# Kernel tuning notes

Measured on AMD Instinct MI355X. Metric: run time of the kernel, lower is better.

The kernel has to match this reference:

```python
import jax, jax.numpy as jnp
import numpy as np
from jax import lax

E = 8      # embed dim
H = 8      # num heads (head_dim = 1)
EPS = 1e-5


def pe_row(pos, d=E):
    # PositionalEncoding quirk: original adds pe[:, x.size(1), :] -> a SINGLE row at index L.
    i = jnp.arange(0, d, 2, dtype=jnp.float32)
    div = jnp.exp(i * (-np.log(10000.0) / d))
    row = jnp.zeros((d,), jnp.float32)
    row = row.at[0::2].set(jnp.sin(pos * div))
    row = row.at[1::2].set(jnp.cos(pos * div))
    return row


def layernorm(x, g, b):
    mu = jnp.mean(x, axis=-1, keepdims=True)
    var = jnp.mean((x - mu) ** 2, axis=-1, keepdims=True)
    return (x - mu) / jnp.sqrt(var + EPS) * g + b


def mha(q, k, v, wi, bi, wo, bo):
    # torch nn.MultiheadAttention, batch_first, eval mode (dropout off)
    d = E // H
    qp = q @ wi[:E].T + bi[:E]
    kp = k @ wi[E:2 * E].T + bi[E:2 * E]
    vp = v @ wi[2 * E:].T + bi[2 * E:]
    sh = lambda x: x.reshape(x.shape[0], x.shape[1], H, d).transpose(0, 2, 1, 3)
    qh, kh, vh = sh(qp), sh(kp), sh(vp)
    scores = jnp.einsum('bhqd,bhkd->bhqk', qh, kh) / np.sqrt(d)
    attn = jax.nn.softmax(scores, axis=-1)
    o = jnp.einsum('bhqk,bhkd->bhqd', attn, vh)
    B, _, L, _ = o.shape
    o = o.transpose(0, 2, 1, 3).reshape(B, L, E)
    return o @ wo.T + bo


def conv1d_k1p1(x, w, b):
    # Conv1d kernel_size=1, padding=1 (conv_tgt branch), then permute to (B, L, C)
    y = lax.conv_general_dilated(x, w, (1,), [(1, 1)],
                                 dimension_numbers=('NCW', 'OIW', 'NCW'))
    return (y + b[None, :, None]).transpose(0, 2, 1)


def setup_inputs() -> dict:
    key = jax.random.key(0)
    ks = jax.random.split(key, 32)
    B = 8192
    r = lambda i, shape, s=0.05: jax.random.normal(ks[i], shape, jnp.float32) * s
    return {
        'eeg': jax.random.normal(ks[0], (B, 2, 20, 118), jnp.float32),
        'pupil': jax.random.normal(ks[1], (B, 2, 30), jnp.float32),
        'speech': jax.random.normal(ks[2], (B, 2, 30), jnp.float32),
        'action': jax.random.normal(ks[3], (B, 2, 30), jnp.float32),
        'location': jax.random.normal(ks[4], (B, 3, 30), jnp.float32),
        'tgt': jax.random.normal(ks[5], (B, 30), jnp.float32),
        'eeg_conv_w': r(6, (E, 2, 20, 2), 0.1), 'eeg_conv_b': r(7, (E,)),
        'psa_conv_w': r(8, (E, 2, 1), 0.3), 'psa_conv_b': r(9, (E,)),
        'loc_conv_w': r(10, (E, 3, 1), 0.3), 'loc_conv_b': r(11, (E,)),
        'tgt_conv_w': r(12, (E, 1, 1), 0.3), 'tgt_conv_b': r(13, (E,)),
        'norm_g': jnp.ones((E,), jnp.float32), 'norm_b': jnp.zeros((E,), jnp.float32),
        'cross_in_w': r(14, (3 * E, E), 0.3), 'cross_in_b': r(15, (3 * E,)),
        'cross_out_w': r(16, (E, E), 0.3), 'cross_out_b': r(17, (E,)),
        'self_in_w': r(18, (3 * E, E), 0.3), 'self_in_b': r(19, (3 * E,)),
        'self_out_w': r(20, (E, E), 0.3), 'self_out_b': r(21, (E,)),
        'out_in_w': r(22, (3 * E, E), 0.3), 'out_in_b': r(23, (3 * E,)),
        'out_out_w': r(24, (E, E), 0.3), 'out_out_b': r(25, (E,)),
        'fc1_w': r(26, (90, 256), 0.1), 'fc1_b': r(27, (90,)),
    }


def reference(eeg, pupil, speech, action, location, tgt,
              eeg_conv_w, eeg_conv_b, psa_conv_w, psa_conv_b,
              loc_conv_w, loc_conv_b, tgt_conv_w, tgt_conv_b,
              norm_g, norm_b,
              cross_in_w, cross_in_b, cross_out_w, cross_out_b,
              self_in_w, self_in_b, self_out_w, self_out_b,
              out_in_w, out_in_b, out_out_w, out_out_b,
              fc1_w, fc1_b):
    B = eeg.shape[0]
    # eeg conv2d: (B,2,20,118) -> (B,8,1,30) -> (B,30,8)
    e = lax.conv_general_dilated(eeg, eeg_conv_w, (1, 4), 'VALID',
                                 dimension_numbers=('NCHW', 'OIHW', 'NCHW'))
    e = (e + eeg_conv_b[None, :, None, None]).squeeze(2).transpose(0, 2, 1)
    # pupil/speech/action/location (raw len 30 -> conv_tgt branch -> seq 32)
    p = conv1d_k1p1(pupil, psa_conv_w, psa_conv_b)
    s = conv1d_k1p1(speech, psa_conv_w, psa_conv_b)
    a = conv1d_k1p1(action, psa_conv_w, psa_conv_b)
    l = conv1d_k1p1(location, loc_conv_w, loc_conv_b)
    # positional encoding adds single row pe[L]
    e = e + pe_row(30.0)
    p = p + pe_row(32.0)
    s = s + pe_row(32.0)
    a = a + pe_row(32.0)
    l = l + pe_row(32.0)

    cross = lambda q, kv: mha(q, kv, kv, cross_in_w, cross_in_b, cross_out_w, cross_out_b)
    selfa = lambda x: mha(x, x, x, self_in_w, self_in_b, self_out_w, self_out_b)
    nrm = lambda x: layernorm(x, norm_g, norm_b)

    eeg_final = (nrm(cross(e, p)) + nrm(cross(e, a)) + nrm(cross(e, l))
                 + nrm(selfa(e)) + nrm(cross(e, s)))
    pupil_final = (nrm(cross(p, e)) + nrm(cross(p, a)) + nrm(cross(p, l))
                   + nrm(selfa(p)) + nrm(cross(p, s)))
    s_cross_l = nrm(cross(s, l))
    speech_final = (nrm(cross(s, e)) + nrm(cross(s, p)) + nrm(cross(s, a))
                    + s_cross_l)  # original omits speech_self
    # original bug: action_cross_location = norm(speech_cross_location)
    action_final = (nrm(cross(a, e)) + nrm(cross(a, p)) + s_cross_l
                    + nrm(selfa(a)) + nrm(cross(a, s)))
    concatenated = jnp.concatenate([eeg_final, pupil_final, action_final, speech_final], axis=1)  # (B,126,8)

    t = conv1d_k1p1(tgt[:, None, :], tgt_conv_w, tgt_conv_b)  # (B,32,8)
    t = t + pe_row(32.0)
    out = mha(t, concatenated, concatenated, out_in_w, out_in_b, out_out_w, out_out_b)  # (B,32,8)
    out = out.reshape(B, 32 * E) @ fc1_w.T + fc1_b  # (B,90)
    out = out.reshape(B, 30, 3).transpose(0, 2, 1)  # (B,3,30)
    return jax.nn.softmax(out, axis=1)
```

## Files before the change

kernel.cpp:

```cpp
#include <hip/hip_runtime.h>
#include <cstdint>
#include <cstddef>

#define NT 256
#define LOG2E 1.4426950408889634f

typedef float v2f __attribute__((ext_vector_type(2)));
typedef float v4f __attribute__((ext_vector_type(4)));

#if defined(__has_builtin)
#  if __has_builtin(__builtin_amdgcn_exp2f)
#    define EXP2F(x) __builtin_amdgcn_exp2f(x)
#  else
#    define EXP2F(x) exp2f(x)
#  endif
#else
#  define EXP2F(x) exp2f(x)
#endif

enum {
  OFF_EEGB = 0,
  OFF_PSAW = 8,
  OFF_PSAB = 24,
  OFF_LOCW = 32,
  OFF_LOCB = 56,
  OFF_TGTW = 64,
  OFF_TGTB = 72,
  OFF_NG   = 80,
  OFF_NB   = 88,
  OFF_CINW = 96,
  OFF_CINB = 288,
  OFF_COUTW= 312,
  OFF_COUTB= 376,
  OFF_SINW = 384,
  OFF_SINB = 576,
  OFF_SOUTW= 600,
  OFF_SOUTB= 664,
  OFF_OINW = 672,
  OFF_OINB = 864,
  OFF_OOUTW= 888,
  OFF_OOUTB= 952,
  OFF_FC1B = 960,
  OFF_PE30 = 1052,
  OFF_PE32 = 1060,
  OFF_Ebuf = 1068,
  OFF_Pbuf = 1308,
  OFF_Sbuf = 1564,
  OFF_Abuf = 1820,
  OFF_Lbuf = 2076,
  OFF_Tbuf = 2332,
  OFF_CAT  = 2588,
  OFF_QP   = 3596,
  OFF_K8   = 4236,
  OFF_V8   = 6540,
  OFF_FCO  = 8844,
  SM_TOTAL = 8936,
  OFF_EEGW = OFF_K8,
  OFF_KF   = OFF_K8,
  OFF_VF   = OFF_K8 + 1056,
};

struct BD { short qoff, Lq, set, sel, dst, flags; };
static __device__ const BD g_bd[18] = {
  {OFF_Ebuf, 30, 1, 0,  0, 1},
  {OFF_Ebuf, 30, 3, 0,  0, 0},
  {OFF_Ebuf, 30, 4, 0,  0, 0},
  {OFF_Ebuf, 30, 5, 1,  0, 0},
  {OFF_Ebuf, 30, 2, 0,  0, 2},
  {OFF_Pbuf, 32, 0, 0, 30, 1},
  {OFF_Pbuf, 32, 3, 0, 30, 0},
  {OFF_Pbuf, 32, 4, 0, 30, 0},
  {OFF_Pbuf, 32, 6, 1, 30, 0},
  {OFF_Pbuf, 32, 2, 0, 30, 2},
  {OFF_Sbuf, 32, 0, 0, 94, 1},
  {OFF_Sbuf, 32, 1, 0, 94, 0},
  {OFF_Sbuf, 32, 3, 0, 94, 0},
  {OFF_Sbuf, 32, 4, 0, 94, 2|4},
  {OFF_Abuf, 32, 0, 0, 62, 1},
  {OFF_Abuf, 32, 1, 0, 62, 0},
  {OFF_Abuf, 32, 2, 0, 62, 0},
  {OFF_Abuf, 32, 7, 1, 62, 2|8},
};

__device__ __forceinline__ float hsum4(v4f a) {
  v2f t = a.xy + a.zw;
  return t.x + t.y;
}

__device__ __forceinline__ float dot8(const float* __restrict__ x,
                                      const float* __restrict__ w, float bias) {
  v4f xa = *(const v4f*)x, xb = *(const v4f*)(x + 4);
  return bias + hsum4(xa * *(const v4f*)w + xb * *(const v4f*)(w + 4));
}

template<int LK>
__device__ __forceinline__ float attn1_nv(float q, const float* Kp, const float* Vp,
                                          float* qslot, int h, const float* sm,
                                          int woutO, int boutO, float gg, float bb) {
  v4f l4 = {0.f,0.f,0.f,0.f}, A4 = {0.f,0.f,0.f,0.f};
  #pragma unroll
  for (int t = 0; t < (LK >> 2); t++) {
    v4f kk = *(const v4f*)(Kp + 4 * t);
    v4f vv = *(const v4f*)(Vp + 4 * t);
    v4f sc = kk * q;
    v4f ee = { EXP2F(sc.x), EXP2F(sc.y), EXP2F(sc.z), EXP2F(sc.w) };
    l4 += ee; A4 += ee * vv;
  }
  if constexpr ((LK & 3) != 0) {
    v2f kk = *(const v2f*)(Kp + (LK & ~3));
    v2f vv = *(const v2f*)(Vp + (LK & ~3));
    v2f sc = kk * q;
    v2f ee = { EXP2F(sc.x), EXP2F(sc.y) };
    l4.xy = l4.xy + ee; A4.xy = A4.xy + ee * vv;
  }
  float ov = hsum4(A4) * __builtin_amdgcn_rcpf(hsum4(l4));
  qslot[h] = ov;
  v4f c0 = *(const v4f*)qslot, c1 = *(const v4f*)(qslot + 4);
  v4f woa = *(const v4f*)(sm + woutO + h * 8), wob = *(const v4f*)(sm + woutO + h * 8 + 4);
  float a = sm[boutO + h] + hsum4(c0 * woa + c1 * wob);
  qslot[h] = a;
  c0 = *(const v4f*)qslot; c1 = *(const v4f*)(qslot + 4);
  float mu = hsum4(c0 + c1) * 0.125f;
  v4f e0 = c0 - mu, e1 = c1 - mu;
  float var = hsum4(e0 * e0 + e1 * e1) * 0.125f;
  return fmaf((a - mu) * rsqrtf(var + 1e-5f), gg, bb);
}

__global__ __launch_bounds__(NT, 4) void cmt_kernel(
    const float* __restrict__ eeg, const float* __restrict__ pupil,
    const float* __restrict__ speech, const float* __restrict__ action,
    const float* __restrict__ location, const float* __restrict__ tgt,
    const float* __restrict__ eeg_w, const float* __restrict__ eeg_b,
    const float* __restrict__ psa_w, const float* __restrict__ psa_b,
    const float* __restrict__ loc_w, const float* __restrict__ loc_b,
    const float* __restrict__ tgt_w, const float* __restrict__ tgt_b,
    const float* __restrict__ ng, const float* __restrict__ nb,
    const float* __restrict__ cin_w, const float* __restrict__ cin_b,
    const float* __restrict__ cout_w, const float* __restrict__ cout_b,
    const float* __restrict__ sin_w, const float* __restrict__ sin_b,
    const float* __restrict__ sout_w, const float* __restrict__ sout_b,
    const float* __restrict__ oin_w, const float* __restrict__ oin_b,
    const float* __restrict__ oout_w, const float* __restrict__ oout_b,
    const float* __restrict__ fc1_w, const float* __restrict__ fc1_b,
    float* __restrict__ out)
{
  __shared__ __align__(16) float sm[SM_TOTAL];
  const int tid = threadIdx.x;
  const int b = blockIdx.x;

#define CP(off, p, n) for (int i = tid; i < (n); i += NT) sm[(off)+i] = (p)[i]
#define CPQ(off, p, n, nq) for (int i = tid; i < (n); i += NT) sm[(off)+i] = (p)[i] * ((i < (nq)) ? LOG2E : 1.0f)

  for (int i = tid; i < 640; i += NT) sm[OFF_EEGW + (i / 80) * 84 + (i % 80)] = eeg_w[i];
  CP(OFF_EEGB, eeg_b, 8);
  CP(OFF_PSAW, psa_w, 16);   CP(OFF_PSAB, psa_b, 8);
  CP(OFF_LOCW, loc_w, 24);   CP(OFF_LOCB, loc_b, 8);
  CP(OFF_TGTW, tgt_w, 8);    CP(OFF_TGTB, tgt_b, 8);
  CP(OFF_NG, ng, 8);         CP(OFF_NB, nb, 8);
  CPQ(OFF_CINW, cin_w, 192, 64);  CPQ(OFF_CINB, cin_b, 24, 8);
  CP(OFF_COUTW, cout_w, 64); CP(OFF_COUTB, cout_b, 8);
  CPQ(OFF_SINW, sin_w, 192, 64);  CPQ(OFF_SINB, sin_b, 24, 8);
  CP(OFF_SOUTW, sout_w, 64); CP(OFF_SOUTB, sout_b, 8);
  CPQ(OFF_OINW, oin_w, 192, 64);  CPQ(OFF_OINB, oin_b, 24, 8);
  CP(OFF_OOUTW, oout_w, 64); CP(OFF_OOUTB, oout_b, 8);
  CP(OFF_FC1B, fc1_b, 90);
  if (tid < 16) {
    const float divs[4] = {1.f, 0.1f, 0.01f, 0.001f};
    float pos = (tid < 8) ? 30.f : 32.f;
    int e = tid & 7;
    float x = pos * divs[e >> 1];
    float v = (e & 1) ? cosf(x) : sinf(x);
    sm[((tid < 8) ? OFF_PE30 : OFF_PE32) + e] = v;
  }
  __syncthreads();

  if (tid < 240) {
    int w = tid >> 3, o = tid & 7;
    const float* ep = eeg + (size_t)b * 4720 + 4 * w;
    const float* wr = sm + OFF_EEGW + o * 84;
    v4f acc4 = {0.f, 0.f, 0.f, 0.f};
    #pragma unroll
    for (int t = 0; t < 20; t++) {
      int ik0 = 2 * t, ik1 = 2 * t + 1;
      float2 x0 = *(const float2*)(ep + (ik0 / 20) * 2360 + (ik0 % 20) * 118);
      float2 x1 = *(const float2*)(ep + (ik1 / 20) * 2360 + (ik1 % 20) * 118);
      v4f xv = {x0.x, x0.y, x1.x, x1.y};
      acc4 += xv * *(const v4f*)(wr + 4 * t);
    }
    sm[OFF_Ebuf + w * 8 + o] = hsum4(acc4) + sm[OFF_EEGB + o] + sm[OFF_PE30 + o];
  }
  {
    int t = tid >> 3, o = tid & 7;
    bool inb = (t >= 1 && t <= 30);
    int ti = t - 1;
    float pe = sm[OFF_PE32 + o];
    float w0 = sm[OFF_PSAW + 2 * o], w1 = sm[OFF_PSAW + 2 * o + 1];
    float pb = sm[OFF_PSAB + o];
    float vp = pb, vs = pb, va = pb;
    float vl = sm[OFF_LOCB + o], vt = sm[OFF_TGTB + o];
    if (inb) {
      const float* pp = pupil    + (size_t)b * 60 + ti;
      const float* sp = speech   + (size_t)b * 60 + ti;
      const float* ap = action   + (size_t)b * 60 + ti;
      const float* lp = location + (size_t)b * 90 + ti;
      vp = fmaf(pp[0], w0, fmaf(pp[30], w1, vp));
      vs = fmaf(sp[0], w0, fmaf(sp[30], w1, vs));
      va = fmaf(ap[0], w0, fmaf(ap[30], w1, va));
      vl = fmaf(lp[0],  sm[OFF_LOCW + 3 * o],     vl);
      vl = fmaf(lp[30], sm[OFF_LOCW + 3 * o + 1], vl);
      vl = fmaf(lp[60], sm[OFF_LOCW + 3 * o + 2], vl);
      vt = fmaf(tgt[(size_t)b * 30 + ti], sm[OFF_TGTW + o], vt);
    }
    sm[OFF_Pbuf + tid] = vp + pe;
    sm[OFF_Sbuf + tid] = vs + pe;
    sm[OFF_Abuf + tid] = va + pe;
    sm[OFF_Lbuf + tid] = vl + pe;
    sm[OFF_Tbuf + tid] = vt + pe;
  }
  __syncthreads();

  const int qi = tid >> 3, h = tid & 7;
  float* qslot = sm + OFF_QP + qi * 20;

  {
    const int r = qi;
    v4f cka = *(const v4f*)(sm + OFF_CINW + 64 + h * 8), ckb = *(const v4f*)(sm + OFF_CINW + 68 + h * 8);
    v4f cva = *(const v4f*)(sm + OFF_CINW + 128 + h * 8), cvb = *(const v4f*)(sm + OFF_CINW + 132 + h * 8);
    float cbk = sm[OFF_CINB + 8 + h], cbv = sm[OFF_CINB + 16 + h];
#define KV1(srcO, set, wka, wkb, wva, wvb, bk, bv) { \
    v4f xa = *(const v4f*)(sm + (srcO) + r * 8); \
    v4f xb = *(const v4f*)(sm + (srcO) + r * 8 + 4); \
    sm[OFF_K8 + (set) * 288 + h * 36 + r] = (bk) + hsum4(xa * (wka) + xb * (wkb)); \
    sm[OFF_V8 + (set) * 288 + h * 36 + r] = (bv) + hsum4(xa * (wva) + xb * (wvb)); }
    if (r < 30) KV1(OFF_Ebuf, 0, cka, ckb, cva, cvb, cbk, cbv);
    KV1(OFF_Pbuf, 1, cka, ckb, cva, cvb, cbk, cbv);
    KV1(OFF_Sbuf, 2, cka, ckb, cva, cvb, cbk, cbv);
    KV1(OFF_Abuf, 3, cka, ckb, cva, cvb, cbk, cbv);
    KV1(OFF_Lbuf, 4, cka, ckb, cva, cvb, cbk, cbv);
    v4f ska = *(const v4f*)(sm + OFF_SINW + 64 + h * 8), skb = *(const v4f*)(sm + OFF_SINW + 68 + h * 8);
    v4f sva = *(const v4f*)(sm + OFF_SINW + 128 + h * 8), svb = *(const v4f*)(sm + OFF_SINW + 132 + h * 8);
    float sbk = sm[OFF_SINB + 8 + h], sbv = sm[OFF_SINB + 16 + h];
    if (r < 30) KV1(OFF_Ebuf, 5, ska, skb, sva, svb, sbk, sbv);
    KV1(OFF_Pbuf, 6, ska, skb, sva, svb, sbk, sbv);
    KV1(OFF_Abuf, 7, ska, skb, sva, svb, sbk, sbv);
#undef KV1
  }
  __syncthreads();

  {
    const float gg = sm[OFF_NG + h], bb = sm[OFF_NB + h];
    float cat = 0.f, carry = 0.f;
    #pragma unroll 1
    for (int mi = 0; mi < 18; mi++) {
      const BD d = g_bd[mi];
      if (qi < d.Lq) {
        const int winO  = d.sel ? OFF_SINW  : OFF_CINW;
        const int binO  = d.sel ? OFF_SINB  : OFF_CINB;
        const int woutO = d.sel ? OFF_SOUTW : OFF_COUTW;
        const int boutO = d.sel ? OFF_SOUTB : OFF_COUTB;
        float q = dot8(sm + d.qoff + qi * 8, sm + winO + h * 8, sm[binO + h]);
        const float* Kp = sm + OFF_K8 + d.set * 288 + h * 36;
        const float* Vp = sm + OFF_V8 + d.set * 288 + h * 36;
        bool lk30 = (d.set == 0) | (d.set == 5);
        float nv = lk30 ? attn1_nv<30>(q, Kp, Vp, qslot, h, sm, woutO, boutO, gg, bb)
                        : attn1_nv<32>(q, Kp, Vp, qslot, h, sm, woutO, boutO, gg, bb);
        if (d.flags & 1) cat = 0.f;
        cat += nv;
        if (d.flags & 4) carry = nv;
        if (d.flags & 8) cat += carry;
        if (d.flags & 2) sm[OFF_CAT + (d.dst + qi) * 8 + h] = cat;
      }
    }
  }
  __syncthreads();

  {
    v4f fka = *(const v4f*)(sm + OFF_OINW + 64 + h * 8), fkb = *(const v4f*)(sm + OFF_OINW + 68 + h * 8);
    v4f fva = *(const v4f*)(sm + OFF_OINW + 128 + h * 8), fvb = *(const v4f*)(sm + OFF_OINW + 132 + h * 8);
    float fbk = sm[OFF_OINB + 8 + h], fbv = sm[OFF_OINB + 16 + h];
    for (int r = qi; r < 126; r += 32) {
      v4f xa = *(const v4f*)(sm + OFF_CAT + r * 8);
      v4f xb = *(const v4f*)(sm + OFF_CAT + r * 8 + 4);
      sm[OFF_KF + h * 132 + r] = fbk + hsum4(xa * fka + xb * fkb);
      sm[OFF_VF + h * 132 + r] = fbv + hsum4(xa * fva + xb * fvb);
    }
  }
  __syncthreads();

  {
    float qf = dot8(sm + OFF_Tbuf + qi * 8, sm + OFF_OINW + h * 8, sm[OFF_OINB + h]);
    const float* Kp = sm + OFF_KF + h * 132;
    const float* Vp = sm + OFF_VF + h * 132;
    v4f l4 = {0.f,0.f,0.f,0.f}, A4 = {0.f,0.f,0.f,0.f};
    #pragma unroll
    for (int t = 0; t < 31; t++) {
      v4f kk = *(const v4f*)(Kp + 4 * t);
      v4f vv = *(const v4f*)(Vp + 4 * t);
      v4f sc = kk * qf;
      v4f ee = { EXP2F(sc.x), EXP2F(sc.y), EXP2F(sc.z), EXP2F(sc.w) };
      l4 += ee; A4 += ee * vv;
    }
    {
      v2f kk = *(const v2f*)(Kp + 124);
      v2f vv = *(const v2f*)(Vp + 124);
      v2f sc = kk * qf;
      v2f ee = { EXP2F(sc.x), EXP2F(sc.y) };
      l4.xy = l4.xy + ee; A4.xy = A4.xy + ee * vv;
    }
    float ov = hsum4(A4) * __builtin_amdgcn_rcpf(hsum4(l4));
    qslot[h] = ov;
    v4f c0 = *(const v4f*)qslot, c1 = *(const v4f*)(qslot + 4);
    v4f woa = *(const v4f*)(sm + OFF_OOUTW + h * 8), wob = *(const v4f*)(sm + OFF_OOUTW + h * 8 + 4);
    float a = sm[OFF_OOUTB + h] + hsum4(c0 * woa + c1 * wob);
    sm[OFF_Tbuf + qi * 8 + h] = a;
  }
  __syncthreads();

  if (tid < 180) {
    int j = tid >> 1, p = tid & 1;
    const v4f* w4 = (const v4f*)(fc1_w + j * 256);
    const v4f* o4 = (const v4f*)(sm + OFF_Tbuf);
    v4f acc4 = {0.f, 0.f, 0.f, 0.f};
    #pragma unroll 8
    for (int c = p; c < 64; c += 2) acc4 += o4[c] * w4[c];
    float acc = hsum4(acc4);
    acc += __shfl_xor(acc, 1);
    if (p == 0) sm[OFF_FCO + j] = acc + sm[OFF_FC1B + j];
  }
  __syncthreads();
  if (tid < 30) {
    float x0 = sm[OFF_FCO + 3 * tid], x1 = sm[OFF_FCO + 3 * tid + 1], x2 = sm[OFF_FCO + 3 * tid + 2];
    float m = fmaxf(x0, fmaxf(x1, x2));
    float e0 = __expf(x0 - m), e1 = __expf(x1 - m), e2 = __expf(x2 - m);
    float inv = __builtin_amdgcn_rcpf(e0 + e1 + e2);
    float* op = out + (size_t)b * 90;
    op[tid]      = e0 * inv;
    op[30 + tid] = e1 * inv;
    op[60 + tid] = e2 * inv;
  }
#undef CP
#undef CPQ
}

extern "C" void kernel_launch(void* const* d_in, const int* in_sizes, int n_in,
                              void* d_out, int out_size, void* d_ws, size_t ws_size,
                              hipStream_t stream) {
  (void)n_in; (void)out_size; (void)d_ws; (void)ws_size;
  int B = in_sizes[0] / 4720;
  cmt_kernel<<<B, NT, 0, stream>>>(
      (const float*)d_in[0],  (const float*)d_in[1],  (const float*)d_in[2],
      (const float*)d_in[3],  (const float*)d_in[4],  (const float*)d_in[5],
      (const float*)d_in[6],  (const float*)d_in[7],  (const float*)d_in[8],
      (const float*)d_in[9],  (const float*)d_in[10], (const float*)d_in[11],
      (const float*)d_in[12], (const float*)d_in[13], (const float*)d_in[14],
      (const float*)d_in[15], (const float*)d_in[16], (const float*)d_in[17],
      (const float*)d_in[18], (const float*)d_in[19], (const float*)d_in[20],
      (const float*)d_in[21], (const float*)d_in[22], (const float*)d_in[23],
      (const float*)d_in[24], (const float*)d_in[25], (const float*)d_in[26],
      (const float*)d_in[27], (const float*)d_in[28], (const float*)d_in[29],
      (float*)d_out);
}
```

Baseline: 276.1 us.

## Batch three queries per K/V set and fold layernorm mean into out-projection

Replaces the table-driven loop over 18 attention blocks with straight-line code that processes the three query sources sharing each cross-attention K/V set together, so K/V loads from LDS are reused across three queries. It also pre-centers the out-projection weights and biases in shared memory so the layernorm mean is zero by construction, removing the mean reduction. The query projections are hoisted and computed once per source. Costs include higher register pressure from three concurrent accumulator sets and extra instruction footprint from full unrolling. Queries past row 30 for eeg are now computed and discarded instead of skipped.

```diff
diff --git a/kernel.cpp b/kernel.cpp
--- a/kernel.cpp
+++ b/kernel.cpp
@@ -60,28 +60,6 @@
   OFF_VF   = OFF_K8 + 1056,
 };
 
-struct BD { short qoff, Lq, set, sel, dst, flags; };
-static __device__ const BD g_bd[18] = {
-  {OFF_Ebuf, 30, 1, 0,  0, 1},
-  {OFF_Ebuf, 30, 3, 0,  0, 0},
-  {OFF_Ebuf, 30, 4, 0,  0, 0},
-  {OFF_Ebuf, 30, 5, 1,  0, 0},
-  {OFF_Ebuf, 30, 2, 0,  0, 2},
-  {OFF_Pbuf, 32, 0, 0, 30, 1},
-  {OFF_Pbuf, 32, 3, 0, 30, 0},
-  {OFF_Pbuf, 32, 4, 0, 30, 0},
-  {OFF_Pbuf, 32, 6, 1, 30, 0},
-  {OFF_Pbuf, 32, 2, 0, 30, 2},
-  {OFF_Sbuf, 32, 0, 0, 94, 1},
-  {OFF_Sbuf, 32, 1, 0, 94, 0},
-  {OFF_Sbuf, 32, 3, 0, 94, 0},
-  {OFF_Sbuf, 32, 4, 0, 94, 2|4},
-  {OFF_Abuf, 32, 0, 0, 62, 1},
-  {OFF_Abuf, 32, 1, 0, 62, 0},
-  {OFF_Abuf, 32, 2, 0, 62, 0},
-  {OFF_Abuf, 32, 7, 1, 62, 2|8},
-};
-
 __device__ __forceinline__ float hsum4(v4f a) {
   v2f t = a.xy + a.zw;
   return t.x + t.y;
@@ -93,10 +71,54 @@
   return bias + hsum4(xa * *(const v4f*)w + xb * *(const v4f*)(w + 4));
 }
 
+__device__ __forceinline__ float fin_nv(float ov, float* qslot, int h,
+                                        const float* sm, int woutO, int boutO,
+                                        float gg, float bb) {
+  qslot[h] = ov;
+  v4f c0 = *(const v4f*)qslot, c1 = *(const v4f*)(qslot + 4);
+  v4f woa = *(const v4f*)(sm + woutO + h * 8), wob = *(const v4f*)(sm + woutO + h * 8 + 4);
+  float a = sm[boutO + h] + hsum4(c0 * woa + c1 * wob);
+  qslot[h] = a;
+  c0 = *(const v4f*)qslot; c1 = *(const v4f*)(qslot + 4);
+  float var = hsum4(c0 * c0 + c1 * c1) * 0.125f;
+  return fmaf(a * rsqrtf(var + 1e-5f), gg, bb);
+}
+
 template<int LK>
-__device__ __forceinline__ float attn1_nv(float q, const float* Kp, const float* Vp,
-                                          float* qslot, int h, const float* sm,
-                                          int woutO, int boutO, float gg, float bb) {
+__device__ __forceinline__ void attn3_core(float qA, float qB, float qC,
+                                           const float* Kp, const float* Vp,
+                                           float& ovA, float& ovB, float& ovC) {
+  v4f lA = {0.f,0.f,0.f,0.f}, AA = lA, lB = lA, AB = lA, lC = lA, AC = lA;
+  #pragma unroll
+  for (int t = 0; t < (LK >> 2); t++) {
+    v4f kk = *(const v4f*)(Kp + 4 * t);
+    v4f vv = *(const v4f*)(Vp + 4 * t);
+    v4f sA = kk * qA, sB = kk * qB, sC = kk * qC;
+    v4f eA = { EXP2F(sA.x), EXP2F(sA.y), EXP2F(sA.z), EXP2F(sA.w) };
+    v4f eB = { EXP2F(sB.x), EXP2F(sB.y), EXP2F(sB.z), EXP2F(sB.w) };
+    v4f eC = { EXP2F(sC.x), EXP2F(sC.y), EXP2F(sC.z), EXP2F(sC.w) };
+    lA += eA; AA += eA * vv;
+    lB += eB; AB += eB * vv;
+    lC += eC; AC += eC * vv;
+  }
+  if constexpr ((LK & 3) != 0) {
+    v2f kk = *(const v2f*)(Kp + (LK & ~3));
+    v2f vv = *(const v2f*)(Vp + (LK & ~3));
+    v2f sA = kk * qA, sB = kk * qB, sC = kk * qC;
+    v2f eA = { EXP2F(sA.x), EXP2F(sA.y) };
+    v2f eB = { EXP2F(sB.x), EXP2F(sB.y) };
+    v2f eC = { EXP2F(sC.x), EXP2F(sC.y) };
+    lA.xy = lA.xy + eA; AA.xy = AA.xy + eA * vv;
+    lB.xy = lB.xy + eB; AB.xy = AB.xy + eB * vv;
+    lC.xy = lC.xy + eC; AC.xy = AC.xy + eC * vv;
+  }
+  ovA = hsum4(AA) * __builtin_amdgcn_rcpf(hsum4(lA));
+  ovB = hsum4(AB) * __builtin_amdgcn_rcpf(hsum4(lB));
+  ovC = hsum4(AC) * __builtin_amdgcn_rcpf(hsum4(lC));
+}
+
+template<int LK>
+__device__ __forceinline__ float attn1_ov(float q, const float* Kp, const float* Vp) {
   v4f l4 = {0.f,0.f,0.f,0.f}, A4 = {0.f,0.f,0.f,0.f};
   #pragma unroll
   for (int t = 0; t < (LK >> 2); t++) {
@@ -113,17 +135,7 @@
     v2f ee = { EXP2F(sc.x), EXP2F(sc.y) };
     l4.xy = l4.xy + ee; A4.xy = A4.xy + ee * vv;
   }
-  float ov = hsum4(A4) * __builtin_amdgcn_rcpf(hsum4(l4));
-  qslot[h] = ov;
-  v4f c0 = *(const v4f*)qslot, c1 = *(const v4f*)(qslot + 4);
-  v4f woa = *(const v4f*)(sm + woutO + h * 8), wob = *(const v4f*)(sm + woutO + h * 8 + 4);
-  float a = sm[boutO + h] + hsum4(c0 * woa + c1 * wob);
-  qslot[h] = a;
-  c0 = *(const v4f*)qslot; c1 = *(const v4f*)(qslot + 4);
-  float mu = hsum4(c0 + c1) * 0.125f;
-  v4f e0 = c0 - mu, e1 = c1 - mu;
-  float var = hsum4(e0 * e0 + e1 * e1) * 0.125f;
-  return fmaf((a - mu) * rsqrtf(var + 1e-5f), gg, bb);
+  return hsum4(A4) * __builtin_amdgcn_rcpf(hsum4(l4));
 }
 
 __global__ __launch_bounds__(NT, 4) void cmt_kernel(
@@ -216,6 +228,29 @@
     sm[OFF_Abuf + tid] = va + pe;
     sm[OFF_Lbuf + tid] = vl + pe;
     sm[OFF_Tbuf + tid] = vt + pe;
+  }
+  if (tid < 64) {
+    int hcol = tid & 7;
+    float s = 0.f;
+    #pragma unroll
+    for (int e = 0; e < 8; e++) s += sm[OFF_COUTW + e * 8 + hcol];
+    float w = sm[OFF_COUTW + tid];
+    float bsum = 0.f;
+    #pragma unroll
+    for (int e = 0; e < 8; e++) bsum += sm[OFF_COUTB + e];
+    sm[OFF_COUTW + tid] = w - s * 0.125f;
+    if (tid < 8) sm[OFF_COUTB + tid] = sm[OFF_COUTB + tid] - bsum * 0.125f;
+  } else if (tid < 128) {
+    int i = tid - 64, hcol = i & 7;
+    float s = 0.f;
+    #pragma unroll
+    for (int e = 0; e < 8; e++) s += sm[OFF_SOUTW + e * 8 + hcol];
+    float w = sm[OFF_SOUTW + i];
+    float bsum = 0.f;
+    #pragma unroll
+    for (int e = 0; e < 8; e++) bsum += sm[OFF_SOUTB + e];
+    sm[OFF_SOUTW + i] = w - s * 0.125f;
+    if (i < 8) sm[OFF_SOUTB + i] = sm[OFF_SOUTB + i] - bsum * 0.125f;
   }
   __syncthreads();
 
@@ -247,31 +282,58 @@
   }
   __syncthreads();
 
+#define KSET(s) (sm + OFF_K8 + (s) * 288 + h * 36)
+#define VSET(s) (sm + OFF_V8 + (s) * 288 + h * 36)
   {
     const float gg = sm[OFF_NG + h], bb = sm[OFF_NB + h];
-    float cat = 0.f, carry = 0.f;
-    #pragma unroll 1
-    for (int mi = 0; mi < 18; mi++) {
-      const BD d = g_bd[mi];
-      if (qi < d.Lq) {
-        const int winO  = d.sel ? OFF_SINW  : OFF_CINW;
-        const int binO  = d.sel ? OFF_SINB  : OFF_CINB;
-        const int woutO = d.sel ? OFF_SOUTW : OFF_COUTW;
-        const int boutO = d.sel ? OFF_SOUTB : OFF_COUTB;
-        float q = dot8(sm + d.qoff + qi * 8, sm + winO + h * 8, sm[binO + h]);
-        const float* Kp = sm + OFF_K8 + d.set * 288 + h * 36;
-        const float* Vp = sm + OFF_V8 + d.set * 288 + h * 36;
-        bool lk30 = (d.set == 0) | (d.set == 5);
-        float nv = lk30 ? attn1_nv<30>(q, Kp, Vp, qslot, h, sm, woutO, boutO, gg, bb)
-                        : attn1_nv<32>(q, Kp, Vp, qslot, h, sm, woutO, boutO, gg, bb);
-        if (d.flags & 1) cat = 0.f;
-        cat += nv;
-        if (d.flags & 4) carry = nv;
-        if (d.flags & 8) cat += carry;
-        if (d.flags & 2) sm[OFF_CAT + (d.dst + qi) * 8 + h] = cat;
-      }
-    }
-  }
+    float qce = dot8(sm + OFF_Ebuf + qi * 8, sm + OFF_CINW + h * 8, sm[OFF_CINB + h]);
+    float qcp = dot8(sm + OFF_Pbuf + qi * 8, sm + OFF_CINW + h * 8, sm[OFF_CINB + h]);
+    float qcs = dot8(sm + OFF_Sbuf + qi * 8, sm + OFF_CINW + h * 8, sm[OFF_CINB + h]);
+    float qca = dot8(sm + OFF_Abuf + qi * 8, sm + OFF_CINW + h * 8, sm[OFF_CINB + h]);
+    float cat_e = 0.f, cat_p = 0.f, cat_s = 0.f, cat_a = 0.f;
+    float ovA, ovB, ovC;
+    attn3_core<30>(qcp, qcs, qca, KSET(0), VSET(0), ovA, ovB, ovC);
+    cat_p += fin_nv(ovA, qslot, h, sm, OFF_COUTW, OFF_COUTB, gg, bb);
+    cat_s += fin_nv(ovB, qslot, h, sm, OFF_COUTW, OFF_COUTB, gg, bb);
+    cat_a += fin_nv(ovC, qslot, h, sm, OFF_COUTW, OFF_COUTB, gg, bb);
+    attn3_core<32>(qce, qcs, qca, KSET(1), VSET(1), ovA, ovB, ovC);
+    cat_e += fin_nv(ovA, qslot, h, sm, OFF_COUTW, OFF_COUTB, gg, bb);
+    cat_s += fin_nv(ovB, qslot, h, sm, OFF_COUTW, OFF_COUTB, gg, bb);
+    cat_a += fin_nv(ovC, qslot, h, sm, OFF_COUTW, OFF_COUTB, gg, bb);
+    attn3_core<32>(qce, qcp, qca, KSET(2), VSET(2), ovA, ovB, ovC);
+    cat_e += fin_nv(ovA, qslot, h, sm, OFF_COUTW, OFF_COUTB, gg, bb);
+    cat_p += fin_nv(ovB, qslot, h, sm, OFF_COUTW, OFF_COUTB, gg, bb);
+    cat_a += fin_nv(ovC, qslot, h, sm, OFF_COUTW, OFF_COUTB, gg, bb);
+    attn3_core<32>(qce, qcp, qcs, KSET(3), VSET(3), ovA, ovB, ovC);
+    cat_e += fin_nv(ovA, qslot, h, sm, OFF_COUTW, OFF_COUTB, gg, bb);
+    cat_p += fin_nv(ovB, qslot, h, sm, OFF_COUTW, OFF_COUTB, gg, bb);
+    cat_s += fin_nv(ovC, qslot, h, sm, OFF_COUTW, OFF_COUTB, gg, bb);
+    attn3_core<32>(qce, qcp, qcs, KSET(4), VSET(4), ovA, ovB, ovC);
+    cat_e += fin_nv(ovA, qslot, h, sm, OFF_COUTW, OFF_COUTB, gg, bb);
+    cat_p += fin_nv(ovB, qslot, h, sm, OFF_COUTW, OFF_COUTB, gg, bb);
+    {
+      float carry = fin_nv(ovC, qslot, h, sm, OFF_COUTW, OFF_COUTB, gg, bb);
+      cat_s += carry; cat_a += carry;
+    }
+    {
+      float qs = dot8(sm + OFF_Ebuf + qi * 8, sm + OFF_SINW + h * 8, sm[OFF_SINB + h]);
+      cat_e += fin_nv(attn1_ov<30>(qs, KSET(5), VSET(5)), qslot, h, sm, OFF_SOUTW, OFF_SOUTB, gg, bb);
+    }
+    {
+      float qs = dot8(sm + OFF_Pbuf + qi * 8, sm + OFF_SINW + h * 8, sm[OFF_SINB + h]);
+      cat_p += fin_nv(attn1_ov<32>(qs, KSET(6), VSET(6)), qslot, h, sm, OFF_SOUTW, OFF_SOUTB, gg, bb);
+    }
+    {
+      float qs = dot8(sm + OFF_Abuf + qi * 8, sm + OFF_SINW + h * 8, sm[OFF_SINB + h]);
+      cat_a += fin_nv(attn1_ov<32>(qs, KSET(7), VSET(7)), qslot, h, sm, OFF_SOUTW, OFF_SOUTB, gg, bb);
+    }
+    if (qi < 30) sm[OFF_CAT + qi * 8 + h] = cat_e;
+    sm[OFF_CAT + (30 + qi) * 8 + h] = cat_p;
+    sm[OFF_CAT + (94 + qi) * 8 + h] = cat_s;
+    sm[OFF_CAT + (62 + qi) * 8 + h] = cat_a;
+  }
+#undef KSET
+#undef VSET
   __syncthreads();
 
   {
```

Result: slower. 378.7 us (+37.1%).
